# Performance work log

Measured on AMD Instinct MI355X. Metric: run time of the kernel, lower is better.

Reference implementation:

```python
import jax, jax.numpy as jnp
from jax import lax
import numpy as np

B, HW = 256, 64          # batch, image side (grayscale)
L, E, K = 32, 64, 8192   # latent_size, embedding_size, num_embeddings
DN = ('NHWC', 'HWIO', 'NHWC')


def setup_inputs() -> dict:
    key = jax.random.key(0)
    ks = jax.random.split(key, 21)
    n = lambda k, shape, s=0.05: (jax.random.normal(k, shape, jnp.float32) * s)
    return {
        'x': jax.random.uniform(ks[0], (B, HW, HW), jnp.float32),
        # encoder convs (SAME, stride 2): 64->32->16->8
        'enc_w1': n(ks[1], (4, 4, 1, 32)),   'enc_b1': jnp.zeros((32,), jnp.float32),
        'enc_w2': n(ks[2], (4, 4, 32, 64)),  'enc_b2': jnp.zeros((64,), jnp.float32),
        'enc_w3': n(ks[3], (4, 4, 64, 128)), 'enc_b3': jnp.zeros((128,), jnp.float32),
        # encoder dense: flatten 8*8*128=8192 -> 512 -> L*E=2048
        'fc_w': n(ks[4], (8192, 512), 0.02), 'fc_b': jnp.zeros((512,), jnp.float32),
        'ffc_w': n(ks[5], (512, L * E), 0.02), 'ffc_b': jnp.zeros((L * E,), jnp.float32),
        # VQ codebook
        'embeds': n(ks[6], (K, E), 0.02),
        # decoder dense: 2048 -> 512, then 1x1x512 feature map
        'dec_fc_w': n(ks[7], (L * E, 512), 0.02), 'dec_fc_b': jnp.zeros((512,), jnp.float32),
        # decoder conv_transpose VALID: 1->4->16->64
        'dec_w1': n(ks[8], (4, 4, 512, 256)),  'dec_b1': jnp.zeros((256,), jnp.float32),
        'dec_w2': n(ks[9], (4, 4, 256, 128)),  'dec_b2': jnp.zeros((128,), jnp.float32),
        'dec_w3': n(ks[10], (4, 4, 128, 1)),   'dec_b3': jnp.zeros((1,), jnp.float32),
    }


def _conv(h, w, b, s):
    return jax.nn.relu(lax.conv_general_dilated(h, w, (s, s), 'SAME', dimension_numbers=DN) + b)


def reference(x, enc_w1, enc_b1, enc_w2, enc_b2, enc_w3, enc_b3,
              fc_w, fc_b, ffc_w, ffc_b, embeds,
              dec_fc_w, dec_fc_b, dec_w1, dec_b1, dec_w2, dec_b2, dec_w3, dec_b3):
    # ---- encoder ----
    h = x[..., None]                                   # (B,64,64,1)
    h = _conv(h, enc_w1, enc_b1, 2)                    # (B,32,32,32)
    h = _conv(h, enc_w2, enc_b2, 2)                    # (B,16,16,64)
    h = _conv(h, enc_w3, enc_b3, 2)                    # (B,8,8,128)
    h = h.reshape(h.shape[0], -1)                      # (B,8192)
    h = jax.nn.relu(h @ fc_w + fc_b)                   # (B,512)
    pred = jax.nn.relu(h @ ffc_w + ffc_b).reshape(-1, L, E)  # (B,L,E)
    # ---- VQ middle: nearest codebook entry (argmin of L2 norm == argmin of squared dist) ----
    d2 = (jnp.sum(pred * pred, axis=-1, keepdims=True)
          - 2.0 * jnp.einsum('ble,ke->blk', pred, embeds)
          + jnp.sum(embeds * embeds, axis=-1))         # (B,L,K)
    classes = jnp.argmin(d2, axis=-1)                  # (B,L) int
    collected = embeds[classes]                        # (B,L,E) gather
    h = collected.reshape(-1, L * E)                   # (B,2048)
    # ---- decoder ----
    h = jax.nn.relu(h @ dec_fc_w + dec_fc_b)           # (B,512)
    h = h[:, None, None, :]                            # (B,1,1,512)
    h = jax.nn.relu(lax.conv_transpose(h, dec_w1, (1, 1), 'VALID', dimension_numbers=DN) + dec_b1)  # (B,4,4,256)
    h = jax.nn.relu(lax.conv_transpose(h, dec_w2, (4, 4), 'VALID', dimension_numbers=DN) + dec_b2)  # (B,16,16,128)
    out = lax.conv_transpose(h, dec_w3, (4, 4), 'VALID', dimension_numbers=DN) + dec_b3             # (B,64,64,1)
    return out  # L2 loss_type: output_t = logits_t
```

## Files before the change

kernel.cpp:

```cpp
#include <hip/hip_runtime.h>
#include <cfloat>


typedef short bf16x8 __attribute__((ext_vector_type(8)));
typedef float f32x4 __attribute__((ext_vector_type(4)));
#define MFMA16(a, b, c) __builtin_amdgcn_mfma_f32_16x16x32_bf16(a, b, c, 0, 0, 0)

__device__ inline unsigned short f2bf(float x) {
  unsigned u = __float_as_uint(x);
  u += 0x7fffu + ((u >> 16) & 1u);
  return (unsigned short)(u >> 16);
}
__device__ inline float bf2f(unsigned short h) {
  return __uint_as_float(((unsigned)h) << 16);
}
__device__ inline void split3v(float v, unsigned short& hb, unsigned short& mb,
                               unsigned short& lb) {
  hb = f2bf(v);
  float r1 = v - bf2f(hb);
  mb = f2bf(r1);
  lb = f2bf(r1 - bf2f(mb));
}

#define PB0 12672
#define PB1 (PB0 + 13056)
#define PB2 (PB1 + 128)
#define PB3 (PB2 + 512)
#define PB4 (PB3 + 2048)
#define PB5 (PB4 + 32)
#define PB6 (PB5 + 4096)
#define PB7 (PB6 + 2048)
__global__ __launch_bounds__(256) void k_prep_early(
    const float* __restrict__ enc_w2, const float* __restrict__ enc_w3,
    const float* __restrict__ embeds, const float* __restrict__ dec_fc_w,
    const float* __restrict__ dec_w2, unsigned short* __restrict__ h1base,
    unsigned short* __restrict__ h2base, unsigned short* __restrict__ Wp2H,
    unsigned short* __restrict__ Wp2M, unsigned short* __restrict__ Wp2L,
    unsigned short* __restrict__ Wp3H, unsigned short* __restrict__ Wp3M,
    unsigned short* __restrict__ Wp3L, unsigned short* __restrict__ eB,
    float* __restrict__ n2, unsigned short* __restrict__ Bp_dfc,
    unsigned short* __restrict__ Bp_d2) {
  int blk = blockIdx.x;
  int t = threadIdx.x;
  if (blk < PB0) {
    int li = blk * 256 + t;
    int bc = li & 8191;
    int rest = li >> 13;
    int i = rest % 132, plane = rest / 132;
    int b = bc >> 5, c = bc & 31;
    int row, col;
    if (i < 34) { row = 0; col = i; }
    else if (i < 68) { row = 33; col = i - 34; }
    else { int j = i - 68; row = 1 + (j >> 1); col = (j & 1) ? 33 : 0; }
    h1base[(size_t)plane * 9469952 + ((size_t)(b * 34 + row) * 34 + col) * 32 + c] = 0;
  } else if (blk < PB1) {
    int li = (blk - PB0) * 256 + t;
    int bc = li & 16383;
    int rest = li >> 14;
    int i = rest % 68, plane = rest / 68;
    int b = bc >> 6, c = bc & 63;
    int row, col;
    if (i < 18) { row = 0; col = i; }
    else if (i < 36) { row = 17; col = i - 18; }
    else { int j = i - 36; row = 1 + (j >> 1); col = (j & 1) ? 17 : 0; }
    h2base[(size_t)plane * 5308416 + ((size_t)(b * 18 + row) * 18 + col) * 64 + c] = 0;
  } else if (blk < PB2) {
    int idx = (blk - PB1) * 256 + t;
    int j = idx & 7, lane = (idx >> 3) & 63, nt = (idx >> 9) & 3, s = idx >> 11;
    int ci = ((lane >> 4) << 3) + j, co = (nt << 4) + (lane & 15);
    unsigned short hb, mb, lb;
    split3v(enc_w2[(s * 32 + ci) * 64 + co], hb, mb, lb);
    Wp2H[idx] = hb; Wp2M[idx] = mb; Wp2L[idx] = lb;
  } else if (blk < PB3) {
    int idx = (blk - PB2) * 256 + t;
    int j = idx & 7, lane = (idx >> 3) & 63, ks = (idx >> 9) & 1;
    int nt = (idx >> 10) & 3, ch = (idx >> 12) & 1, s = idx >> 13;
    int ci = ks * 32 + ((lane >> 4) << 3) + j;
    int co = ch * 64 + (nt << 4) + (lane & 15);
    unsigned short hb, mb, lb;
    split3v(enc_w3[(s * 64 + ci) * 128 + co], hb, mb, lb);
    Wp3H[idx] = hb; Wp3M[idx] = mb; Wp3L[idx] = lb;
  } else if (blk < PB4) {
    int idx = (blk - PB3) * 256 + t;
    int j = idx & 7, lane = (idx >> 3) & 63;
    int f = idx >> 9;
    int nt = f & 3, ks = (f >> 2) & 1, kt = f >> 3;
    int code = kt * 64 + nt * 16 + (lane & 15);
    int k = ks * 32 + ((lane >> 4) << 3) + j;
    unsigned short hb, mb, lb;
    split3v(embeds[(size_t)code * 64 + k], hb, mb, lb);
    size_t base = (size_t)f * 1536 + lane * 8 + j;
    eB[base] = hb; eB[base + 512] = mb; eB[base + 1024] = lb;
  } else if (blk < PB5) {
    int k = (blk - PB4) * 256 + t;
    const float4* p = (const float4*)(embeds + (size_t)k * 64);
    float s0 = 0, s1 = 0, s2 = 0, s3 = 0;
#pragma unroll
    for (int j = 0; j < 16; ++j) {
      float4 v = p[j];
      s0 = fmaf(v.x, v.x, s0); s1 = fmaf(v.y, v.y, s1);
      s2 = fmaf(v.z, v.z, s2); s3 = fmaf(v.w, v.w, s3);
    }
    n2[k] = (s0 + s1) + (s2 + s3);
  } else if (blk < PB6) {
    int idx = (blk - PB5) * 256 + t;
    int j = idx & 7, lane = (idx >> 3) & 63;
    int f = idx >> 9;
    int ntg = f & 31;
    int kt = f >> 5;
    int k = kt * 32 + ((lane >> 4) << 3) + j;
    int n = ntg * 16 + (lane & 15);
    unsigned short hb, mb, lb;
    split3v(dec_fc_w[(size_t)k * 512 + n], hb, mb, lb);
    Bp_dfc[idx] = hb; Bp_dfc[idx + 1048576] = mb;
  } else if (blk < PB7) {
    int idx = (blk - PB6) * 256 + t;
    int j = idx & 7, lane = (idx >> 3) & 63;
    int f = idx >> 9;
    int ntg = f & 127;
    int kt = f >> 7;
    int k = kt * 32 + ((lane >> 4) << 3) + j;
    int n = ntg * 16 + (lane & 15);
    int o = n & 127, ru = n >> 7;
    int r = ru >> 2, u = ru & 3;
    int sf = (3 - r) * 4 + (3 - u);
    unsigned short hb, mb, lb;
    split3v(dec_w2[(((size_t)sf * 256 + k) << 7) + o], hb, mb, lb);
    Bp_d2[idx] = hb; Bp_d2[idx + 524288] = mb;
  }
}

__global__ __launch_bounds__(256) void k_conv1(const float* __restrict__ x,
                                               const float* __restrict__ w,
                                               const float* __restrict__ bias,
                                               unsigned short* __restrict__ oH,
                                               unsigned short* __restrict__ oM,
                                               unsigned short* __restrict__ oL) {
  int b = blockIdx.x >> 5;
  int y = blockIdx.x & 31;
  int t = threadIdx.x;
  int c = t & 31;
  int xg = t >> 5;
  float acc[4] = {0.f, 0.f, 0.f, 0.f};
  for (int dy = 0; dy < 4; ++dy) {
    int iy = 2 * y + dy - 1;
    if (iy < 0 || iy >= 64) continue;
    const float* xrow = x + ((size_t)b * 64 + iy) * 64;
    for (int dx = 0; dx < 4; ++dx) {
      float wv = w[(dy * 4 + dx) * 32 + c];
#pragma unroll
      for (int i = 0; i < 4; ++i) {
        int ix = 8 * xg + 2 * i + dx - 1;
        float v = (ix >= 0 && ix < 64) ? xrow[ix] : 0.f;
        acc[i] = fmaf(v, wv, acc[i]);
      }
    }
  }
  float bv = bias[c];
#pragma unroll
  for (int i = 0; i < 4; ++i) {
    float v = acc[i] + bv;
    v = v > 0.f ? v : 0.f;
    unsigned short hb, mb, lb;
    split3v(v, hb, mb, lb);
    size_t o = ((size_t)(b * 34 + y + 1) * 34 + (4 * xg + i + 1)) * 32 + c;
    oH[o] = hb; oM[o] = mb; oL[o] = lb;
  }
}

__global__ __launch_bounds__(1024, 4) void k_conv2s(
    const unsigned short* __restrict__ aH, const unsigned short* __restrict__ aM,
    const unsigned short* __restrict__ aL, const unsigned short* __restrict__ wH,
    const unsigned short* __restrict__ wM, const unsigned short* __restrict__ wL,
    const float* __restrict__ bias, unsigned short* __restrict__ oH,
    unsigned short* __restrict__ oM, unsigned short* __restrict__ oL) {
  __shared__ unsigned short Bs[49152];
  int t = threadIdx.x;
  int wave = t >> 6, lane = t & 63;
  int l15 = lane & 15, quad = lane >> 4;
  int m0 = blockIdx.x * 256 + wave * 16;
  int p = m0 + l15;
  int b = p >> 8, y = (p >> 4) & 15, x = p & 15;
  f32x4 acc[4] = {};
#pragma unroll
  for (int hf = 0; hf < 2; ++hf) {
    if (hf) __syncthreads();
    {
      const unsigned short* s0 = wH + hf * 16384;
      const unsigned short* s1 = wM + hf * 16384;
      const unsigned short* s2 = wL + hf * 16384;
#pragma unroll
      for (int i = 0; i < 2; ++i) {
        int o8 = (i * 1024 + t) * 8;
        *(bf16x8*)(Bs + o8)         = *(const bf16x8*)(s0 + o8);
        *(bf16x8*)(Bs + 16384 + o8) = *(const bf16x8*)(s1 + o8);
        *(bf16x8*)(Bs + 32768 + o8) = *(const bf16x8*)(s2 + o8);
      }
    }
    __syncthreads();
#pragma unroll 4
    for (int sl = 0; sl < 8; ++sl) {
      int s = hf * 8 + sl;
      int dy = s >> 2, dx = s & 3;
      size_t aoff = ((size_t)(b * 34 + 2 * y + dy) * 34 + (2 * x + dx)) * 32 + quad * 8;
      bf16x8 ah = *(const bf16x8*)(aH + aoff);
      bf16x8 am = *(const bf16x8*)(aM + aoff);
      bf16x8 al = *(const bf16x8*)(aL + aoff);
#pragma unroll
      for (int nt = 0; nt < 4; ++nt) {
        const unsigned short* bp = Bs + ((sl * 4 + nt) * 64 + lane) * 8;
        bf16x8 bh = *(const bf16x8*)(bp);
        bf16x8 bm = *(const bf16x8*)(bp + 16384);
        bf16x8 bl = *(const bf16x8*)(bp + 32768);
        acc[nt] = MFMA16(am, bm, acc[nt]);
        acc[nt] = MFMA16(ah, bl, acc[nt]);
        acc[nt] = MFMA16(al, bh, acc[nt]);
        acc[nt] = MFMA16(ah, bm, acc[nt]);
        acc[nt] = MFMA16(am, bh, acc[nt]);
        acc[nt] = MFMA16(ah, bh, acc[nt]);
      }
    }
  }
#pragma unroll
  for (int r = 0; r < 4; ++r) {
    int pp = m0 + quad * 4 + r;
    int b2 = pp >> 8, yo = (pp >> 4) & 15, xo = pp & 15;
    size_t obase = ((size_t)(b2 * 18 + yo + 1) * 18 + (xo + 1)) * 64;
#pragma unroll
    for (int nt = 0; nt < 4; ++nt) {
      int co = nt * 16 + l15;
      float v = acc[nt][r] + bias[co];
      v = v > 0.f ? v : 0.f;
      unsigned short hb, mb, lb;
      split3v(v, hb, mb, lb);
      oH[obase + co] = hb; oM[obase + co] = mb; oL[obase + co] = lb;
    }
  }
}

__global__ __launch_bounds__(512, 2) void k_conv3s(
    const unsigned short* __restrict__ aH, const unsigned short* __restrict__ aM,
    const unsigned short* __restrict__ aL, const unsigned short* __restrict__ wH,
    const unsigned short* __restrict__ wM, const unsigned short* __restrict__ wL,
    float* __restrict__ part) {
  __shared__ unsigned short Bs[2][24576];
  int t = threadIdx.x;
  int wave = t >> 6, lane = t & 63;
  int l15 = lane & 15, quad = lane >> 4;
  int ch = wave & 1, mg = wave >> 1;
  int m0 = blockIdx.x * 128 + mg * 32;
  int z = blockIdx.y;
  f32x4 acc[2][4] = {};
  {
    const unsigned short* srcH = wH + (size_t)(z * 8) * 8192;
    const unsigned short* srcM = wM + (size_t)(z * 8) * 8192;
    const unsigned short* srcL = wL + (size_t)(z * 8) * 8192;
#pragma unroll
    for (int i = 0; i < 2; ++i) {
      int o8 = (i * 512 + t) * 8;
      *(bf16x8*)(&Bs[0][o8])         = *(const bf16x8*)(srcH + o8);
      *(bf16x8*)(&Bs[0][8192 + o8])  = *(const bf16x8*)(srcM + o8);
      *(bf16x8*)(&Bs[0][16384 + o8]) = *(const bf16x8*)(srcL + o8);
    }
  }
  __syncthreads();
#pragma unroll 2
  for (int si = 0; si < 8; ++si) {
    int s = z * 8 + si;
    int cur = si & 1, nxt = cur ^ 1;
    bf16x8 stg[6];
    if (si < 7) {
      const unsigned short* srcH = wH + (size_t)(s + 1) * 8192;
      const unsigned short* srcM = wM + (size_t)(s + 1) * 8192;
      const unsigned short* srcL = wL + (size_t)(s + 1) * 8192;
#pragma unroll
      for (int i = 0; i < 2; ++i) {
        int o8 = (i * 512 + t) * 8;
        stg[i]     = *(const bf16x8*)(srcH + o8);
        stg[2 + i] = *(const bf16x8*)(srcM + o8);
        stg[4 + i] = *(const bf16x8*)(srcL + o8);
      }
    }
    int dy = s >> 2, dx = s & 3;
    bf16x8 ah[2][2], am[2][2], al[2][2];
#pragma unroll
    for (int mt = 0; mt < 2; ++mt) {
      int p = m0 + mt * 16 + l15;
      int b = p >> 6, y = (p >> 3) & 7, x = p & 7;
      size_t base = ((size_t)(b * 18 + 2 * y + dy) * 18 + (2 * x + dx)) * 64 + quad * 8;
#pragma unroll
      for (int ks = 0; ks < 2; ++ks) {
        ah[mt][ks] = *(const bf16x8*)(aH + base + ks * 32);
        am[mt][ks] = *(const bf16x8*)(aM + base + ks * 32);
        al[mt][ks] = *(const bf16x8*)(aL + base + ks * 32);
      }
    }
#pragma unroll
    for (int nt = 0; nt < 4; ++nt)
#pragma unroll
      for (int ks = 0; ks < 2; ++ks) {
        const unsigned short* bp =
            &Bs[cur][((ch * 4 + nt) * 2 + ks) * 512 + lane * 8];
        bf16x8 bh = *(const bf16x8*)(bp);
        bf16x8 bm = *(const bf16x8*)(bp + 8192);
        bf16x8 bl = *(const bf16x8*)(bp + 16384);
#pragma unroll
        for (int mt = 0; mt < 2; ++mt) {
          acc[mt][nt] = MFMA16(am[mt][ks], bm, acc[mt][nt]);
          acc[mt][nt] = MFMA16(ah[mt][ks], bl, acc[mt][nt]);
          acc[mt][nt] = MFMA16(al[mt][ks], bh, acc[mt][nt]);
          acc[mt][nt] = MFMA16(ah[mt][ks], bm, acc[mt][nt]);
          acc[mt][nt] = MFMA16(am[mt][ks], bh, acc[mt][nt]);
          acc[mt][nt] = MFMA16(ah[mt][ks], bh, acc[mt][nt]);
        }
      }
    if (si < 7) {
#pragma unroll
      for (int i = 0; i < 2; ++i) {
        int o8 = (i * 512 + t) * 8;
        *(bf16x8*)(&Bs[nxt][o8])         = stg[i];
        *(bf16x8*)(&Bs[nxt][8192 + o8])  = stg[2 + i];
        *(bf16x8*)(&Bs[nxt][16384 + o8]) = stg[4 + i];
      }
    }
    __syncthreads();
  }
  float* Cp = part + (size_t)z * 2097152;
#pragma unroll
  for (int mt = 0; mt < 2; ++mt)
#pragma unroll
    for (int nt = 0; nt < 4; ++nt) {
      int co = ch * 64 + nt * 16 + l15;
#pragma unroll
      for (int r = 0; r < 4; ++r) {
        int pp = m0 + mt * 16 + quad * 4 + r;
        Cp[(size_t)pp * 128 + co] = acc[mt][nt][r];
      }
    }
}

#define FB0 8192
#define FB1 (FB0 + 16384)
__global__ __launch_bounds__(256) void k_prep_fc(
    const float* __restrict__ part, const float* __restrict__ enc_b3,
    unsigned short* __restrict__ h3H, unsigned short* __restrict__ h3M,
    unsigned short* __restrict__ h3L, const float* __restrict__ fc_w,
    unsigned short* __restrict__ Bp_fc) {
  int blk = blockIdx.x;
  int t = threadIdx.x;
  if (blk < FB0) {
    int idx = blk * 256 + t;
    float s = part[idx] + part[2097152 + idx] + enc_b3[idx & 127];
    s = s > 0.f ? s : 0.f;
    unsigned short hb, mb, lb;
    split3v(s, hb, mb, lb);
    h3H[idx] = hb; h3M[idx] = mb; h3L[idx] = lb;
  } else {
    int idx = (blk - FB0) * 256 + t;
    int j = idx & 7, lane = (idx >> 3) & 63;
    int f = idx >> 9;
    int ntg = f & 31;
    int kt = f >> 5;
    int k = kt * 32 + ((lane >> 4) << 3) + j;
    int n = ntg * 16 + (lane & 15);
    unsigned short hb, mb, lb;
    split3v(fc_w[(size_t)k * 512 + n], hb, mb, lb);
    Bp_fc[idx] = hb; Bp_fc[idx + 4194304] = mb; Bp_fc[idx + 8388608] = lb;
  }
}

#define WB0 4096
#define WB1 (WB0 + 8192)
__global__ __launch_bounds__(256) void k_prep_w2(
    const float* __restrict__ ffc_w, unsigned short* __restrict__ Bp_ffc,
    const float* __restrict__ dec_w1, unsigned short* __restrict__ Bp_d1) {
  int blk = blockIdx.x;
  int t = threadIdx.x;
  if (blk < WB0) {
    int idx = blk * 256 + t;
    int j = idx & 7, lane = (idx >> 3) & 63;
    int f = idx >> 9;
    int ntg = f & 127;
    int kt = f >> 7;
    int k = kt * 32 + ((lane >> 4) << 3) + j;
    int n = ntg * 16 + (lane & 15);
    unsigned short hb, mb, lb;
    split3v(ffc_w[(size_t)k * 2048 + n], hb, mb, lb);
    Bp_ffc[idx] = hb; Bp_ffc[idx + 1048576] = mb; Bp_ffc[idx + 2097152] = lb;
  } else {
    int idx = (blk - WB0) * 256 + t;
    int j = idx & 7, lane = (idx >> 3) & 63;
    int f = idx >> 9;
    int ntg = f & 255;
    int kt = f >> 8;
    int k = kt * 32 + ((lane >> 4) << 3) + j;
    int n = ntg * 16 + (lane & 15);
    int o = n & 255, ru = n >> 8;
    int r = ru >> 2, u = ru & 3;
    int sf = (3 - r) * 4 + (3 - u);
    unsigned short hb, mb, lb;
    split3v(dec_w1[(((size_t)sf * 512 + k) << 8) + o], hb, mb, lb);
    Bp_d1[idx] = hb; Bp_d1[idx + 2097152] = mb;
  }
}

template <int NP, int NTW>
__global__ __launch_bounds__(256) void k_mgemm(
    const unsigned short* __restrict__ A0, const unsigned short* __restrict__ A1,
    const unsigned short* __restrict__ A2, const unsigned short* __restrict__ Bp,
    float* __restrict__ C, const float* __restrict__ bias,
    int M, int N, int K, int bmask) {
  int S = gridDim.z;
  int Kc = K / S;
  int t = threadIdx.x;
  int wave = t >> 6, lane = t & 63;
  int l15 = lane & 15, quad = lane >> 4;
  int m0 = blockIdx.x * 64 + wave * 16;
  int n0 = blockIdx.y * (16 * NTW);
  int KT = K >> 5, NT = N >> 4;
  int kt0 = (blockIdx.z * Kc) >> 5;
  int ktn = Kc >> 5;
  size_t sstride = (size_t)KT * NT * 512;
  const unsigned short* arow0 = A0 + (size_t)(m0 + l15) * K + quad * 8;
  const unsigned short* arow1 = A1 + (size_t)(m0 + l15) * K + quad * 8;
  const unsigned short* arow2 = nullptr;
  if constexpr (NP == 3) arow2 = A2 + (size_t)(m0 + l15) * K + quad * 8;
  f32x4 acc[NTW] = {};
  for (int kt = kt0; kt < kt0 + ktn; ++kt) {
    bf16x8 ah = *(const bf16x8*)(arow0 + kt * 32);
    bf16x8 am = *(const bf16x8*)(arow1 + kt * 32);
    bf16x8 al;
    if constexpr (NP == 3) al = *(const bf16x8*)(arow2 + kt * 32);
    const unsigned short* bbase =
        Bp + ((size_t)kt * NT + (n0 >> 4)) * 512 + lane * 8;
#pragma unroll
    for (int nt = 0; nt < NTW; ++nt) {
      const unsigned short* bp = bbase + nt * 512;
      bf16x8 bh = *(const bf16x8*)(bp);
      bf16x8 bm = *(const bf16x8*)(bp + sstride);
      if constexpr (NP == 3) {
        bf16x8 bl = *(const bf16x8*)(bp + 2 * sstride);
        acc[nt] = MFMA16(am, bm, acc[nt]);
        acc[nt] = MFMA16(ah, bl, acc[nt]);
        acc[nt] = MFMA16(al, bh, acc[nt]);
        acc[nt] = MFMA16(ah, bm, acc[nt]);
        acc[nt] = MFMA16(am, bh, acc[nt]);
        acc[nt] = MFMA16(ah, bh, acc[nt]);
      } else {
        acc[nt] = MFMA16(ah, bm, acc[nt]);
        acc[nt] = MFMA16(am, bh, acc[nt]);
        acc[nt] = MFMA16(ah, bh, acc[nt]);
      }
    }
  }
  if (S == 1) {
#pragma unroll
    for (int nt = 0; nt < NTW; ++nt) {
      int n = n0 + nt * 16 + l15;
      float bv = bias[n & bmask];
#pragma unroll
      for (int r = 0; r < 4; ++r) {
        int m = m0 + quad * 4 + r;
        float v = acc[nt][r] + bv;
        C[(size_t)m * N + n] = v > 0.f ? v : 0.f;
      }
    }
  } else {
    float* Cp = C + (size_t)blockIdx.z * M * N;
#pragma unroll
    for (int nt = 0; nt < NTW; ++nt) {
      int n = n0 + nt * 16 + l15;
#pragma unroll
      for (int r = 0; r < 4; ++r) {
        int m = m0 + quad * 4 + r;
        Cp[(size_t)m * N + n] = acc[nt][r];
      }
    }
  }
}

template <int NPOUT>
__global__ __launch_bounds__(256) void k_sumrelu3(
    const float* __restrict__ part, const float* __restrict__ bias,
    unsigned short* __restrict__ oH, unsigned short* __restrict__ oM,
    unsigned short* __restrict__ oL, int MN, int bmask, int S) {
  int idx = blockIdx.x * 256 + threadIdx.x;
  float s = 0.f;
  for (int z = 0; z < S; ++z) s += part[(size_t)z * MN + idx];
  s += bias[idx & bmask];
  s = s > 0.f ? s : 0.f;
  unsigned short hb = f2bf(s);
  float r1 = s - bf2f(hb);
  unsigned short mb = f2bf(r1);
  oH[idx] = hb; oM[idx] = mb;
  if constexpr (NPOUT == 3) oL[idx] = f2bf(r1 - bf2f(mb));
}

__global__ __launch_bounds__(256, 2) void k_vqmfma3(
    const unsigned short* __restrict__ pH, const unsigned short* __restrict__ pM,
    const unsigned short* __restrict__ pL, const unsigned short* __restrict__ eB,
    const float* __restrict__ n2, float* __restrict__ pbd, int* __restrict__ pbk) {
  __shared__ unsigned short Es[2][12288];
  int t = threadIdx.x;
  int wave = t >> 6, lane = t & 63;
  int l15 = lane & 15, quad = lane >> 4;
  int m0 = blockIdx.x * 128 + wave * 32;
  int z = blockIdx.y;
  bf16x8 ah[2][2], am[2][2], al[2][2];
#pragma unroll
  for (int mt = 0; mt < 2; ++mt) {
    size_t arow = (size_t)(m0 + mt * 16 + l15) * 64 + quad * 8;
#pragma unroll
    for (int ks = 0; ks < 2; ++ks) {
      ah[mt][ks] = *(const bf16x8*)(pH + arow + ks * 32);
      am[mt][ks] = *(const bf16x8*)(pM + arow + ks * 32);
      al[mt][ks] = *(const bf16x8*)(pL + arow + ks * 32);
    }
  }
  float bd[2][4]; int bk[2][4];
#pragma unroll
  for (int mt = 0; mt < 2; ++mt)
#pragma unroll
    for (int r = 0; r < 4; ++r) { bd[mt][r] = FLT_MAX; bk[mt][r] = 0; }
  {
    const unsigned short* src = eB + (size_t)(z * 16) * 12288;
#pragma unroll
    for (int i = 0; i < 6; ++i) {
      int o8 = (i * 256 + t) * 8;
      *(bf16x8*)(&Es[0][o8]) = *(const bf16x8*)(src + o8);
    }
  }
  __syncthreads();
  for (int ki = 0; ki < 16; ++ki) {
    int kt = z * 16 + ki;
    int cur = ki & 1, nxt = cur ^ 1;
    bf16x8 stg[6];
    if (ki < 15) {
      const unsigned short* src = eB + (size_t)(kt + 1) * 12288;
#pragma unroll
      for (int i = 0; i < 6; ++i) {
        int o8 = (i * 256 + t) * 8;
        stg[i] = *(const bf16x8*)(src + o8);
      }
    }
    const unsigned short* bb = &Es[cur][lane * 8];
    f32x4 acc[2][4] = {};
#pragma unroll
    for (int ks = 0; ks < 2; ++ks)
#pragma unroll
      for (int nt = 0; nt < 4; ++nt) {
        const unsigned short* bp = bb + ((ks * 4 + nt) * 3) * 512;
        bf16x8 bh = *(const bf16x8*)(bp);
        bf16x8 bm = *(const bf16x8*)(bp + 512);
        bf16x8 bl = *(const bf16x8*)(bp + 1024);
#pragma unroll
        for (int mt = 0; mt < 2; ++mt) {
          acc[mt][nt] = MFMA16(am[mt][ks], bm, acc[mt][nt]);
          acc[mt][nt] = MFMA16(ah[mt][ks], bl, acc[mt][nt]);
          acc[mt][nt] = MFMA16(al[mt][ks], bh, acc[mt][nt]);
          acc[mt][nt] = MFMA16(ah[mt][ks], bm, acc[mt][nt]);
          acc[mt][nt] = MFMA16(am[mt][ks], bh, acc[mt][nt]);
          acc[mt][nt] = MFMA16(ah[mt][ks], bh, acc[mt][nt]);
        }
      }
    int cb = kt * 64;
#pragma unroll
    for (int nt = 0; nt < 4; ++nt) {
      int code = cb + nt * 16 + l15;
      float nv = n2[code];
#pragma unroll
      for (int mt = 0; mt < 2; ++mt)
#pragma unroll
        for (int r = 0; r < 4; ++r) {
          float d = fmaf(-2.f, acc[mt][nt][r], nv);
          if (d < bd[mt][r]) { bd[mt][r] = d; bk[mt][r] = code; }
        }
    }
    if (ki < 15) {
#pragma unroll
      for (int i = 0; i < 6; ++i) {
        int o8 = (i * 256 + t) * 8;
        *(bf16x8*)(&Es[nxt][o8]) = stg[i];
      }
    }
    __syncthreads();
  }
#pragma unroll
  for (int mt = 0; mt < 2; ++mt)
#pragma unroll
    for (int r = 0; r < 4; ++r)
#pragma unroll
      for (int s = 1; s < 16; s <<= 1) {
        float od = __shfl_xor(bd[mt][r], s);
        int ok = __shfl_xor(bk[mt][r], s);
        if (od < bd[mt][r] || (od == bd[mt][r] && ok < bk[mt][r])) {
          bd[mt][r] = od; bk[mt][r] = ok;
        }
      }
  if (l15 == 0) {
#pragma unroll
    for (int mt = 0; mt < 2; ++mt)
#pragma unroll
      for (int r = 0; r < 4; ++r) {
        pbd[(size_t)z * 8192 + m0 + mt * 16 + quad * 4 + r] = bd[mt][r];
        pbk[(size_t)z * 8192 + m0 + mt * 16 + quad * 4 + r] = bk[mt][r];
      }
  }
}

__global__ __launch_bounds__(256) void k_vqgather(const float* __restrict__ pbd,
                                                  const int* __restrict__ pbk,
                                                  const float* __restrict__ embeds,
                                                  unsigned short* __restrict__ cH,
                                                  unsigned short* __restrict__ cM) {
  int idx = blockIdx.x * 256 + threadIdx.x;
  int m = idx >> 6;
  float bd = pbd[m]; int bk = pbk[m];
#pragma unroll
  for (int z = 1; z < 8; ++z) {
    float d = pbd[(size_t)z * 8192 + m]; int k = pbk[(size_t)z * 8192 + m];
    if (d < bd || (d == bd && k < bk)) { bd = d; bk = k; }
  }
  float v = embeds[(size_t)bk * 64 + (idx & 63)];
  unsigned short hb = f2bf(v);
  cH[idx] = hb;
  cM[idx] = f2bf(v - bf2f(hb));
}

__global__ __launch_bounds__(256) void k_dec3(const float* __restrict__ d2buf,
                                              const float* __restrict__ w3,
                                              const float* __restrict__ b3,
                                              float* __restrict__ out) {
  __shared__ float sx[16 * 129];
  __shared__ float wT[128 * 16];
  int b = blockIdx.x >> 4;
  int y = blockIdx.x & 15;
  int t = threadIdx.x;
#pragma unroll
  for (int j = 0; j < 8; ++j) {
    int idx = t + j * 256;
    int xx = idx >> 7, c = idx & 127;
    size_t m2 = ((size_t)b * 4 + (y >> 2)) * 4 + (xx >> 2);
    sx[xx * 129 + c] = d2buf[m2 * 2048 + ((y & 3) * 4 + (xx & 3)) * 128 + c];
  }
#pragma unroll
  for (int j = 0; j < 8; ++j) {
    int idx = t + j * 256;
    int c = idx >> 4, ru = idx & 15;
    int R = ru >> 2, U = ru & 3;
    wT[c * 16 + ru] = w3[((3 - R) * 4 + (3 - U)) * 128 + c];
  }
  __syncthreads();
  int xx = t >> 4, ru = t & 15;
  float a0 = 0, a1 = 0, a2 = 0, a3 = 0;
#pragma unroll 8
  for (int c = 0; c < 128; c += 4) {
    a0 = fmaf(sx[xx * 129 + c + 0], wT[(c + 0) * 16 + ru], a0);
    a1 = fmaf(sx[xx * 129 + c + 1], wT[(c + 1) * 16 + ru], a1);
    a2 = fmaf(sx[xx * 129 + c + 2], wT[(c + 2) * 16 + ru], a2);
    a3 = fmaf(sx[xx * 129 + c + 3], wT[(c + 3) * 16 + ru], a3);
  }
  float acc = (a0 + a1) + (a2 + a3) + b3[0];
  int R = ru >> 2, U = ru & 3;
  out[((size_t)b * 64 + 4 * y + R) * 64 + 4 * xx + U] = acc;
}

extern "C" void kernel_launch(void* const* d_in, const int* in_sizes, int n_in,
                              void* d_out, int out_size, void* d_ws, size_t ws_size,
                              hipStream_t stream) {
  const float* x        = (const float*)d_in[0];
  const float* enc_w1   = (const float*)d_in[1];
  const float* enc_b1   = (const float*)d_in[2];
  const float* enc_w2   = (const float*)d_in[3];
  const float* enc_b2   = (const float*)d_in[4];
  const float* enc_w3   = (const float*)d_in[5];
  const float* enc_b3   = (const float*)d_in[6];
  const float* fc_w     = (const float*)d_in[7];
  const float* fc_b     = (const float*)d_in[8];
  const float* ffc_w    = (const float*)d_in[9];
  const float* ffc_b    = (const float*)d_in[10];
  const float* embeds   = (const float*)d_in[11];
  const float* dec_fc_w = (const float*)d_in[12];
  const float* dec_fc_b = (const float*)d_in[13];
  const float* dec_w1   = (const float*)d_in[14];
  const float* dec_b1   = (const float*)d_in[15];
  const float* dec_w2   = (const float*)d_in[16];
  const float* dec_b2   = (const float*)d_in[17];
  const float* dec_w3   = (const float*)d_in[18];
  const float* dec_b3   = (const float*)d_in[19];
  float* outp = (float*)d_out;

  char* ws = (char*)d_ws;
  size_t off = 0;
  auto alloc = [&](size_t bytes) { size_t r = off; off = (off + bytes + 255) & ~(size_t)255; return r; };

  size_t RA = alloc(57147392);
  unsigned short* h1pH = (unsigned short*)(ws + RA);
  unsigned short* h1pM = (unsigned short*)(ws + RA + 18939904);
  unsigned short* h1pL = (unsigned short*)(ws + RA + 37879808);
  float* d2buf            = (float*)(ws + RA);
  float* partials         = (float*)(ws + RA + 33554432);
  unsigned short* Bp_d1   = (unsigned short*)(ws + RA + 41943040);
  unsigned short* d1H     = (unsigned short*)(ws + RA + 50331648);
  unsigned short* d1M     = (unsigned short*)(ws + RA + 52428800);
  unsigned short* hdH     = (unsigned short*)(ws + RA + 54525952);
  unsigned short* hdM     = (unsigned short*)(ws + RA + 54788096);
  unsigned short* cH      = (unsigned short*)(ws + RA + 55050240);
  unsigned short* cM      = (unsigned short*)(ws + RA + 56098816);

  size_t RB = alloc(31850496);
  unsigned short* h2pH = (unsigned short*)(ws + RB);
  unsigned short* h2pM = (unsigned short*)(ws + RB + 10616832);
  unsigned short* h2pL = (unsigned short*)(ws + RB + 21233664);
  unsigned short* Bp_fc = (unsigned short*)(ws + RB);
  unsigned short* pH    = (unsigned short*)(ws + RB + 28311552);
  unsigned short* pM    = (unsigned short*)(ws + RB + 29360128);
  unsigned short* pL    = (unsigned short*)(ws + RB + 30408704);

  size_t RC = alloc(12582912);
  unsigned short* h3H = (unsigned short*)(ws + RC);
  unsigned short* h3M = (unsigned short*)(ws + RC + 4194304);
  unsigned short* h3L = (unsigned short*)(ws + RC + 8388608);
  unsigned short* Bp_ffc = (unsigned short*)(ws + RC);
  unsigned short* hfcH   = (unsigned short*)(ws + RC + 6291456);
  unsigned short* hfcM   = (unsigned short*)(ws + RC + 6553600);
  unsigned short* hfcL   = (unsigned short*)(ws + RC + 6815744);

  unsigned short* eB     = (unsigned short*)(ws + alloc(3145728));
  unsigned short* Bp_dfc = (unsigned short*)(ws + alloc(4194304));
  unsigned short* Bp_d2  = (unsigned short*)(ws + alloc(2097152));
  float* n2buf   = (float*)(ws + alloc(32768));
  float* pbd     = (float*)(ws + alloc(262144));
  int*   pbk     = (int*)  (ws + alloc(262144));
  unsigned short* Wp2H = (unsigned short*)(ws + alloc(196608));
  unsigned short* Wp2M = Wp2H + 32768;
  unsigned short* Wp2L = Wp2M + 32768;
  unsigned short* Wp3H = (unsigned short*)(ws + alloc(786432));
  unsigned short* Wp3M = Wp3H + 131072;
  unsigned short* Wp3L = Wp3M + 131072;
  (void)ws_size; (void)in_sizes; (void)n_in; (void)out_size;

  k_prep_early<<<PB7, 256, 0, stream>>>(
      enc_w2, enc_w3, embeds, dec_fc_w, dec_w2, h1pH, h2pH,
      Wp2H, Wp2M, Wp2L, Wp3H, Wp3M, Wp3L, eB, n2buf, Bp_dfc, Bp_d2);

  k_conv1<<<8192, 256, 0, stream>>>(x, enc_w1, enc_b1, h1pH, h1pM, h1pL);
  k_conv2s<<<256, 1024, 0, stream>>>(h1pH, h1pM, h1pL, Wp2H, Wp2M, Wp2L,
                                     enc_b2, h2pH, h2pM, h2pL);
  k_conv3s<<<dim3(128, 2), 512, 0, stream>>>(h2pH, h2pM, h2pL,
                                             Wp3H, Wp3M, Wp3L, partials);
  k_prep_fc<<<FB1, 256, 0, stream>>>(partials, enc_b3, h3H, h3M, h3L,
                                     fc_w, Bp_fc);

  k_mgemm<3, 4><<<dim3(4, 8, 16), 256, 0, stream>>>(
      h3H, h3M, h3L, Bp_fc, partials, fc_b, 256, 512, 8192, 511);
  k_prep_w2<<<WB1, 256, 0, stream>>>(ffc_w, Bp_ffc, dec_w1, Bp_d1);
  k_sumrelu3<3><<<512, 256, 0, stream>>>(partials, fc_b, hfcH, hfcM, hfcL,
                                         131072, 511, 16);
  k_mgemm<3, 4><<<dim3(4, 32, 4), 256, 0, stream>>>(
      hfcH, hfcM, hfcL, Bp_ffc, partials, ffc_b, 256, 2048, 512, 2047);
  k_sumrelu3<3><<<2048, 256, 0, stream>>>(partials, ffc_b, pH, pM, pL,
                                          524288, 2047, 4);

  k_vqmfma3<<<dim3(64, 8), 256, 0, stream>>>(pH, pM, pL, eB, n2buf, pbd, pbk);
  k_vqgather<<<2048, 256, 0, stream>>>(pbd, pbk, embeds, cH, cM);

  k_mgemm<2, 4><<<dim3(4, 8, 16), 256, 0, stream>>>(
      cH, cM, nullptr, Bp_dfc, partials, dec_fc_b, 256, 512, 2048, 511);
  k_sumrelu3<2><<<512, 256, 0, stream>>>(partials, dec_fc_b, hdH, hdM, nullptr,
                                         131072, 511, 16);

  k_mgemm<2, 4><<<dim3(4, 64, 2), 256, 0, stream>>>(
      hdH, hdM, nullptr, Bp_d1, partials, dec_b1, 256, 4096, 512, 255);
  k_sumrelu3<2><<<4096, 256, 0, stream>>>(partials, dec_b1, d1H, d1M, nullptr,
                                          1048576, 255, 2);

  k_mgemm<2, 8><<<dim3(64, 16, 1), 256, 0, stream>>>(
      d1H, d1M, nullptr, Bp_d2, d2buf, dec_b2, 4096, 2048, 256, 127);

  k_dec3<<<4096, 256, 0, stream>>>(d2buf, dec_w3, dec_b3, outp);
}
```

Baseline: 425.7 us.

## Double-buffer conv2 weights via async global-to-LDS loads with 2 M-tiles per wave

Rewrites the second encoder conv kernel to use 512 threads where each wave computes two 16-row M tiles, reusing each LDS weight fragment across both. Weights are staged in four quarters into a double-buffered LDS array using global_load_lds, so the next quarter loads while the current one is consumed. This is meant to hide weight staging latency and halve LDS weight reads per MFMA, at the cost of more registers per wave and fewer waves per block.

```diff
diff --git a/kernel.cpp b/kernel.cpp
--- a/kernel.cpp
+++ b/kernel.cpp
@@ -168,74 +168,91 @@
   }
 }
 
-__global__ __launch_bounds__(1024, 4) void k_conv2s(
+__global__ __launch_bounds__(512, 2) void k_conv2q(
     const unsigned short* __restrict__ aH, const unsigned short* __restrict__ aM,
     const unsigned short* __restrict__ aL, const unsigned short* __restrict__ wH,
     const unsigned short* __restrict__ wM, const unsigned short* __restrict__ wL,
     const float* __restrict__ bias, unsigned short* __restrict__ oH,
     unsigned short* __restrict__ oM, unsigned short* __restrict__ oL) {
-  __shared__ unsigned short Bs[49152];
+  __shared__ unsigned short Bs[2][24576];
   int t = threadIdx.x;
   int wave = t >> 6, lane = t & 63;
   int l15 = lane & 15, quad = lane >> 4;
-  int m0 = blockIdx.x * 256 + wave * 16;
-  int p = m0 + l15;
-  int b = p >> 8, y = (p >> 4) & 15, x = p & 15;
-  f32x4 acc[4] = {};
-#pragma unroll
-  for (int hf = 0; hf < 2; ++hf) {
-    if (hf) __syncthreads();
-    {
-      const unsigned short* s0 = wH + hf * 16384;
-      const unsigned short* s1 = wM + hf * 16384;
-      const unsigned short* s2 = wL + hf * 16384;
-#pragma unroll
-      for (int i = 0; i < 2; ++i) {
-        int o8 = (i * 1024 + t) * 8;
-        *(bf16x8*)(Bs + o8)         = *(const bf16x8*)(s0 + o8);
-        *(bf16x8*)(Bs + 16384 + o8) = *(const bf16x8*)(s1 + o8);
-        *(bf16x8*)(Bs + 32768 + o8) = *(const bf16x8*)(s2 + o8);
+  int m0 = blockIdx.x * 256 + wave * 32;
+  auto stage_async = [&](int q, int buf) {
+    const unsigned short* s0 = wH + q * 8192;
+    const unsigned short* s1 = wM + q * 8192;
+    const unsigned short* s2 = wL + q * 8192;
+#pragma unroll
+    for (int i = 0; i < 2; ++i) {
+      int coff = (i * 8 + wave) * 512;
+      __builtin_amdgcn_global_load_lds(
+          (const __attribute__((address_space(1))) void*)(s0 + coff + lane * 8),
+          (__attribute__((address_space(3))) void*)(&Bs[buf][coff]), 16, 0, 0);
+      __builtin_amdgcn_global_load_lds(
+          (const __attribute__((address_space(1))) void*)(s1 + coff + lane * 8),
+          (__attribute__((address_space(3))) void*)(&Bs[buf][8192 + coff]), 16, 0, 0);
+      __builtin_amdgcn_global_load_lds(
+          (const __attribute__((address_space(1))) void*)(s2 + coff + lane * 8),
+          (__attribute__((address_space(3))) void*)(&Bs[buf][16384 + coff]), 16, 0, 0);
+    }
+  };
+  f32x4 acc[2][4] = {};
+  stage_async(0, 0);
+  __syncthreads();
+  for (int q = 0; q < 4; ++q) {
+    int cur = q & 1;
+    if (q < 3) stage_async(q + 1, cur ^ 1);
+#pragma unroll
+    for (int sl = 0; sl < 4; ++sl) {
+      int s = q * 4 + sl;
+      int dy = s >> 2, dx = s & 3;
+      bf16x8 ah[2], am[2], al[2];
+#pragma unroll
+      for (int mt = 0; mt < 2; ++mt) {
+        int p = m0 + mt * 16 + l15;
+        int b = p >> 8, y = (p >> 4) & 15, x = p & 15;
+        size_t aoff = ((size_t)(b * 34 + 2 * y + dy) * 34 + (2 * x + dx)) * 32 + quad * 8;
+        ah[mt] = *(const bf16x8*)(aH + aoff);
+        am[mt] = *(const bf16x8*)(aM + aoff);
+        al[mt] = *(const bf16x8*)(aL + aoff);
+      }
+#pragma unroll
+      for (int nt = 0; nt < 4; ++nt) {
+        const unsigned short* bp = &Bs[cur][(sl * 4 + nt) * 512 + lane * 8];
+        bf16x8 bh = *(const bf16x8*)(bp);
+        bf16x8 bm = *(const bf16x8*)(bp + 8192);
+        bf16x8 bl = *(const bf16x8*)(bp + 16384);
+#pragma unroll
+        for (int mt = 0; mt < 2; ++mt) {
+          acc[mt][nt] = MFMA16(am[mt], bm, acc[mt][nt]);
+          acc[mt][nt] = MFMA16(ah[mt], bl, acc[mt][nt]);
+          acc[mt][nt] = MFMA16(al[mt], bh, acc[mt][nt]);
+          acc[mt][nt] = MFMA16(ah[mt], bm, acc[mt][nt]);
+          acc[mt][nt] = MFMA16(am[mt], bh, acc[mt][nt]);
+          acc[mt][nt] = MFMA16(ah[mt], bh, acc[mt][nt]);
+        }
       }
     }
     __syncthreads();
-#pragma unroll 4
-    for (int sl = 0; sl < 8; ++sl) {
-      int s = hf * 8 + sl;
-      int dy = s >> 2, dx = s & 3;
-      size_t aoff = ((size_t)(b * 34 + 2 * y + dy) * 34 + (2 * x + dx)) * 32 + quad * 8;
-      bf16x8 ah = *(const bf16x8*)(aH + aoff);
-      bf16x8 am = *(const bf16x8*)(aM + aoff);
-      bf16x8 al = *(const bf16x8*)(aL + aoff);
+  }
+#pragma unroll
+  for (int mt = 0; mt < 2; ++mt)
+#pragma unroll
+    for (int r = 0; r < 4; ++r) {
+      int pp = m0 + mt * 16 + quad * 4 + r;
+      int b2 = pp >> 8, yo = (pp >> 4) & 15, xo = pp & 15;
+      size_t obase = ((size_t)(b2 * 18 + yo + 1) * 18 + (xo + 1)) * 64;
 #pragma unroll
       for (int nt = 0; nt < 4; ++nt) {
-        const unsigned short* bp = Bs + ((sl * 4 + nt) * 64 + lane) * 8;
-        bf16x8 bh = *(const bf16x8*)(bp);
-        bf16x8 bm = *(const bf16x8*)(bp + 16384);
-        bf16x8 bl = *(const bf16x8*)(bp + 32768);
-        acc[nt] = MFMA16(am, bm, acc[nt]);
-        acc[nt] = MFMA16(ah, bl, acc[nt]);
-        acc[nt] = MFMA16(al, bh, acc[nt]);
-        acc[nt] = MFMA16(ah, bm, acc[nt]);
-        acc[nt] = MFMA16(am, bh, acc[nt]);
-        acc[nt] = MFMA16(ah, bh, acc[nt]);
-      }
-    }
-  }
-#pragma unroll
-  for (int r = 0; r < 4; ++r) {
-    int pp = m0 + quad * 4 + r;
-    int b2 = pp >> 8, yo = (pp >> 4) & 15, xo = pp & 15;
-    size_t obase = ((size_t)(b2 * 18 + yo + 1) * 18 + (xo + 1)) * 64;
-#pragma unroll
-    for (int nt = 0; nt < 4; ++nt) {
-      int co = nt * 16 + l15;
-      float v = acc[nt][r] + bias[co];
-      v = v > 0.f ? v : 0.f;
-      unsigned short hb, mb, lb;
-      split3v(v, hb, mb, lb);
-      oH[obase + co] = hb; oM[obase + co] = mb; oL[obase + co] = lb;
-    }
-  }
+        int co = nt * 16 + l15;
+        float v = acc[mt][nt][r] + bias[co];
+        v = v > 0.f ? v : 0.f;
+        unsigned short hb, mb, lb;
+        split3v(v, hb, mb, lb);
+        oH[obase + co] = hb; oM[obase + co] = mb; oL[obase + co] = lb;
+      }
+    }
 }
 
 __global__ __launch_bounds__(512, 2) void k_conv3s(
@@ -745,8 +762,8 @@
       Wp2H, Wp2M, Wp2L, Wp3H, Wp3M, Wp3L, eB, n2buf, Bp_dfc, Bp_d2);
 
   k_conv1<<<8192, 256, 0, stream>>>(x, enc_w1, enc_b1, h1pH, h1pM, h1pL);
-  k_conv2s<<<256, 1024, 0, stream>>>(h1pH, h1pM, h1pL, Wp2H, Wp2M, Wp2L,
-                                     enc_b2, h2pH, h2pM, h2pL);
+  k_conv2q<<<256, 512, 0, stream>>>(h1pH, h1pM, h1pL, Wp2H, Wp2M, Wp2L,
+                                    enc_b2, h2pH, h2pM, h2pL);
   k_conv3s<<<dim3(128, 2), 512, 0, stream>>>(h2pH, h2pM, h2pL,
                                              Wp3H, Wp3M, Wp3L, partials);
   k_prep_fc<<<FB1, 256, 0, stream>>>(partials, enc_b3, h3H, h3M, h3L,
```

Result: no change. 432.9 us (+1.7%).
